# Optimization experiments

Measured on AMD Instinct MI355X. Metric: run time of the kernel, lower is better.

The kernel has to match this reference:

```python
import jax, jax.numpy as jnp
import numpy as np
from jax import lax

T = 131072  # num frames
PARENTS = [-1, 0, 0, 1, 2, 3, 4, 5, 6]          # lower-body kinematic tree
LOWER_BODY = [0, 1, 2, 4, 5, 7, 8, 10, 11]      # SMPL joint ids of the 9 lower-body joints
FEET = [7, 5, 8, 6]                              # left toe, left heel, right toe, right heel (lower-body local ids)
FLOOR_Y = -0.93                                  # min y of ankle/foot joints in SMPL zero pose
GRAVITY_VELOCITY = -0.0018


def setup_inputs() -> dict:
    key = jax.random.key(0)
    k1, k2, k3 = jax.random.split(key, 3)
    pose = jax.random.normal(k1, (T, 24, 3, 3), dtype=jnp.float32)
    bone = 0.2 * jax.random.normal(k2, (9, 3), dtype=jnp.float32)
    bone = bone.at[:3].set(0.0)  # root + hip offsets zeroed, as in __init__ (b[:3] = 0)
    index = jax.random.randint(k3, (T,), 0, 4, dtype=jnp.int32)
    return {"pose": pose, "lower_body_bone": bone, "index": index}


def _forward_kinematics(pose_lower, bone):
    # pose_lower: [T, 9, 3, 3] local rotations; bone: [9, 3] bone offsets.
    # R_global[i] = R_global[parent] @ R_local[i];  p[i] = p[parent] + R_global[parent] @ bone[i]
    Rg = [pose_lower[:, 0]]
    p = [jnp.broadcast_to(bone[0], (pose_lower.shape[0], 3))]
    for i in range(1, 9):
        pa = PARENTS[i]
        Rg.append(jnp.einsum('tij,tjk->tik', Rg[pa], pose_lower[:, i]))
        p.append(p[pa] + jnp.einsum('tij,j->ti', Rg[pa], bone[i]))
    return jnp.stack(p, axis=1)  # [T, 9, 3]


def reference(pose, lower_body_bone, index):
    gravity = jnp.array([0.0, GRAVITY_VELOCITY, 0.0], dtype=pose.dtype)
    pose_lower = pose[:, jnp.array(LOWER_BODY)]               # [T, 9, 3, 3]
    j = _forward_kinematics(pose_lower, lower_body_bone)      # [T, 9, 3]

    # per-foot velocities: j[t-1] - j[t], zero at t=0  -> [T, 4, 3]
    feet = j[:, jnp.array(FEET)]                              # [T, 4, 3]
    vel_full = jnp.concatenate([jnp.zeros((1, 4, 3), dtype=j.dtype), feet[:-1] - feet[1:]], axis=0)
    vel_select = jnp.take_along_axis(vel_full, index[:, None, None].astype(jnp.int32), axis=1)[:, 0]  # [T, 3]
    velocity = gravity + vel_select                           # [T, 3]

    # sequential floor-contact correction on the y component
    foot_min_y = jnp.min(j[:, 5:9, 1], axis=1)                # [T]

    def step(root_y, inp):
        vy, fmin = inp
        foot_y = root_y + fmin
        vy_new = jnp.where(foot_y + vy <= FLOOR_Y, FLOOR_Y - foot_y, vy)
        return root_y + vy_new, vy_new

    _, vy_all = lax.scan(step, jnp.asarray(0.0, dtype=j.dtype), (velocity[:, 1], foot_min_y))
    velocity = velocity.at[:, 1].set(vy_all)

    trans = jnp.cumsum(velocity, axis=0)                      # velocity_to_root_position
    return pose, trans
```

## Files before the change

kernel.cpp:

```cpp
#include <hip/hip_runtime.h>
#include <math.h>

#define T_TOTAL   131072
#define POSE_FLTS (131072 * 216)
#define BT        64
#define NU        (T_TOTAL / BT)
#define F4PB      (BT * 54)
#define TS_STR    73
#define TILE_F    72
#define FLOOR_YC  (-0.93f)
#define GRAV_Y    (-0.0018f)
#define NEG_INF   (-INFINITY)

typedef float floatx4 __attribute__((ext_vector_type(4)));


__device__ __forceinline__ void mat3mul(const float* A, const float* B, float* C) {
#pragma unroll
    for (int r = 0; r < 3; ++r) {
#pragma unroll
        for (int c = 0; c < 3; ++c) {
            C[r * 3 + c] = fmaf(A[r * 3 + 2], B[6 + c],
                           fmaf(A[r * 3 + 1], B[3 + c],
                                A[r * 3 + 0] * B[c]));
        }
    }
}

__device__ __forceinline__ void mva(const float* R, const float* b,
                                    const float* pin, float* pout) {
#pragma unroll
    for (int r = 0; r < 3; ++r) {
        pout[r] = pin[r] + fmaf(R[r * 3 + 2], b[2],
                            fmaf(R[r * 3 + 1], b[1], R[r * 3 + 0] * b[0]));
    }
}

__device__ __forceinline__ float sel_foot(const float f[12], int idx, int c) {
    float r = f[0 + c];
    r = (idx == 1) ? f[3 + c] : r;
    r = (idx == 2) ? f[6 + c] : r;
    r = (idx == 3) ? f[9 + c] : r;
    return r;
}

__device__ __forceinline__ void fk_core(const float* Pl,
                                        const float* __restrict__ bone,
                                        float feet[12], float* fmin) {
    const float* M0 = Pl + 0;
    const float* M1 = Pl + 9;
    const float* M2 = Pl + 18;
    const float* M3 = Pl + 28;
    const float* M4 = Pl + 37;
    const float* M5 = Pl + 51;
    const float* M6 = Pl + 60;

    float R1[9], R2[9], R3[9], R4[9], R5[9], R6[9];
    mat3mul(M0, M1, R1);
    mat3mul(M0, M2, R2);
    mat3mul(R1, M3, R3);
    mat3mul(R2, M4, R4);
    mat3mul(R3, M5, R5);
    mat3mul(R4, M6, R6);

    float p0[3] = {bone[0], bone[1], bone[2]};
    float p1[3], p2[3], p3[3], p4a[3], p5[3], p6[3], p7[3], p8[3];
    mva(M0, bone + 3,  p0, p1);
    mva(M0, bone + 6,  p0, p2);
    mva(R1, bone + 9,  p1, p3);
    mva(R2, bone + 12, p2, p4a);
    mva(R3, bone + 15, p3, p5);
    mva(R4, bone + 18, p4a, p6);
    mva(R5, bone + 21, p5, p7);
    mva(R6, bone + 24, p6, p8);

    feet[0] = p7[0]; feet[1]  = p7[1]; feet[2]  = p7[2];
    feet[3] = p5[0]; feet[4]  = p5[1]; feet[5]  = p5[2];
    feet[6] = p8[0]; feet[7]  = p8[1]; feet[8]  = p8[2];
    feet[9] = p6[0]; feet[10] = p6[1]; feet[11] = p6[2];
    *fmin = fminf(fminf(p5[1], p6[1]), fminf(p7[1], p8[1]));
}

__device__ __forceinline__ void fk_feet_col(const float* __restrict__ tile, int col,
                                            const float* __restrict__ bone,
                                            float feet[12], float* fmin) {
    float Pl[TILE_F];
    const float* p = tile + col * TS_STR;
#pragma unroll
    for (int f = 0; f < TILE_F; ++f) Pl[f] = p[f];
    fk_core(Pl, bone, feet, fmin);
}

__device__ __forceinline__ void wave_incl_scan(float& Sx, float& Sz,
                                               float& A, float& B, int lane) {
#pragma unroll
    for (int off = 1; off < 64; off <<= 1) {
        float ox = __shfl_up(Sx, off, 64);
        float oz = __shfl_up(Sz, off, 64);
        float oA = __shfl_up(A, off, 64);
        float oB = __shfl_up(B, off, 64);
        if (lane >= off) {
            Sx += ox;
            Sz += oz;
            B = fmaxf(oB + A, B);
            A = oA + A;
        }
    }
}

__device__ __forceinline__ void extract_tile(float* __restrict__ tile, int idx, floatx4 q) {
    int tsl = idx / 54;
    int w   = idx - tsl * 54;
    int base = -1;
    if (w <= 6)                  base = 4 * w;
    else if (w >= 9 && w <= 13)  base = 4 * w - 8;
    else if (w >= 15 && w <= 20) base = 4 * w - 12;
    if (base >= 0) {
        float* p = &tile[tsl * TS_STR + base];
        p[0] = q.x; p[1] = q.y; p[2] = q.z; p[3] = q.w;
    }
}


__global__ __launch_bounds__(256) void k_main(const float* __restrict__ pose,
                                              const float* __restrict__ bone,
                                              const int* __restrict__ index,
                                              floatx4* __restrict__ outPose4,
                                              float4* __restrict__ vws,
                                              float4* __restrict__ wsAgg) {
    __shared__ __align__(16) float tile[65 * TS_STR + 4];
    int tid = threadIdx.x, u = blockIdx.x;

    const floatx4* __restrict__ src = (const floatx4*)pose + (size_t)u * F4PB;
    floatx4*       __restrict__ dst = outPose4              + (size_t)u * F4PB;

    floatx4 r[14];
#pragma unroll
    for (int j = 0; j < 13; ++j) r[j] = src[j * 256 + tid];
    floatx4 qb;
    bool has14  = (tid < 128);
    bool hasBnd = (u > 0 && tid >= 128 && tid < 128 + 18);
    if (has14) {
        r[13] = src[13 * 256 + tid];
    } else if (hasBnd) {
        int k = tid - 128;
        int o = k + (k >= 7 ? 2 : 0) + (k >= 12 ? 1 : 0);
        qb = *(const floatx4*)(pose + ((size_t)u * BT - 1) * 216 + o * 4);
    }
    int idxv = 0;
    if (tid < 64) idxv = index[u * BT + tid];

#pragma unroll
    for (int j = 0; j < 13; ++j) {
        int idx = j * 256 + tid;
        __builtin_nontemporal_store(r[j], &dst[idx]);
        extract_tile(tile, idx, r[j]);
    }
    if (has14) {
        int idx = 13 * 256 + tid;
        __builtin_nontemporal_store(r[13], &dst[idx]);
        extract_tile(tile, idx, r[13]);
    } else if (hasBnd) {
        int k = tid - 128;
        float* p = &tile[64 * TS_STR + 4 * k];
#pragma unroll
        for (int i = 0; i < 4; ++i) p[i] = qb[i];
    }
    __syncthreads();

    if (tid < 64) {
        int lane = tid;
        int t = u * BT + lane;

        float feet[12], fmin;
        fk_feet_col(tile, lane, bone, feet, &fmin);

        float fb[12];
        if (lane == 0 && u > 0) {
            float mb;
            fk_feet_col(tile, 64, bone, fb, &mb);
        }

        float fp[12];
#pragma unroll
        for (int k = 0; k < 12; ++k) fp[k] = __shfl_up(feet[k], 1, 64);
        if (lane == 0 && u > 0) {
#pragma unroll
            for (int k = 0; k < 12; ++k) fp[k] = fb[k];
        }

        float vx, vy, vz;
        if (t == 0) {
            vx = 0.f; vy = GRAV_Y; vz = 0.f;
        } else {
            vx = sel_foot(fp, idxv, 0) - sel_foot(feet, idxv, 0);
            vy = GRAV_Y + sel_foot(fp, idxv, 1) - sel_foot(feet, idxv, 1);
            vz = sel_foot(fp, idxv, 2) - sel_foot(feet, idxv, 2);
        }
        float ix = vx, iz = vz, iA = vy, iB = FLOOR_YC - fmin;
        wave_incl_scan(ix, iz, iA, iB, lane);

        vws[(size_t)t] = make_float4(ix, iz, iA, iB);
        if (lane == 63) wsAgg[u] = make_float4(ix, iz, iA, iB);
    }
}


__global__ __launch_bounds__(256) void k_apply(const float4* __restrict__ wsAgg,
                                               const float4* __restrict__ vws,
                                               float* __restrict__ trans) {
    __shared__ float4 wtot[4];
    __shared__ float4 pre[4];
    int tid = threadIdx.x, bk = blockIdx.x;
    int lane = tid & 63, wv = tid >> 6;

    float4 a[8];
#pragma unroll
    for (int k = 0; k < 8; ++k) a[k] = wsAgg[tid * 8 + k];
    float cx = a[0].x, cz = a[0].y, ca = a[0].z, cb = a[0].w;
#pragma unroll
    for (int k = 1; k < 8; ++k) {
        cb = fmaxf(cb + a[k].z, a[k].w);
        ca += a[k].z;
        cx += a[k].x; cz += a[k].y;
    }

    float sx = cx, sz = cz, sa = ca, sb = cb;
    wave_incl_scan(sx, sz, sa, sb, lane);
    if (lane == 63) wtot[wv] = make_float4(sx, sz, sa, sb);

    float ex = __shfl_up(sx, 1, 64);
    float ez = __shfl_up(sz, 1, 64);
    float eA = __shfl_up(sa, 1, 64);
    float eB = __shfl_up(sb, 1, 64);
    if (lane == 0) { ex = 0.f; ez = 0.f; eA = 0.f; eB = NEG_INF; }
    __syncthreads();

    float wx = 0.f, wz = 0.f, wA = 0.f, wB = NEG_INF;
    for (int w = 0; w < wv; ++w) {
        float4 c = wtot[w];
        wx += c.x; wz += c.y;
        wB = fmaxf(wB + c.z, c.w);
        wA += c.z;
    }
    float tx = wx + ex, tz = wz + ez;
    float tB = fmaxf(wB + eA, eB);
    float tA = wA + eA;

    if (tid == (bk >> 1)) {
        int j0 = bk * 4 - tid * 8;
        float px = tx, pz = tz, pA = tA, pB = tB;
#pragma unroll
        for (int k = 0; k < 8; ++k) {
            if (k >= j0 && k < j0 + 4)
                pre[k - j0] = make_float4(px, pz, fmaxf(pA, pB), 0.f);
            pB = fmaxf(pB + a[k].z, a[k].w);
            pA += a[k].z;
            px += a[k].x; pz += a[k].y;
        }
    }
    __syncthreads();

    float4 bin = pre[wv];
    size_t t = ((size_t)bk * 4 + wv) * 64 + lane;
    float4 v = vws[t];
    trans[t * 3 + 0] = bin.x + v.x;
    trans[t * 3 + 1] = fmaxf(bin.z + v.z, v.w);
    trans[t * 3 + 2] = bin.y + v.y;
}


extern "C" void kernel_launch(void* const* d_in, const int* in_sizes, int n_in,
                              void* d_out, int out_size, void* d_ws, size_t ws_size,
                              hipStream_t stream) {
    const float* pose  = (const float*)d_in[0];
    const float* bone  = (const float*)d_in[1];
    const int*   index = (const int*)d_in[2];
    float* out   = (float*)d_out;
    float* trans = out + POSE_FLTS;

    float4* vws   = (float4*)d_ws;
    float4* wsAgg = vws + T_TOTAL;
    (void)ws_size; (void)n_in; (void)in_sizes; (void)out_size;

    k_main <<<NU, 256, 0, stream>>>(pose, bone, index, (floatx4*)out, vws, wsAgg);
    k_apply<<<NU / 4, 256, 0, stream>>>(wsAgg, vws, trans);
}
```

Before: 48.77 us.

## Specialize warps: copy waves stream pose, compute wave loads FK data directly

Splits each block into a copy role (three waves streaming the pose block to the output with nontemporal stores) and a compute role (one wave that loads its frame's 18 needed float4s straight from global memory and runs forward kinematics plus the wave scan). This removes the shared-memory tile, the extract scatter and the block barrier. In exchange the compute wave reads pose data a second time with strided per-lane 16-byte loads that are poorly coalesced, relying on cache hits. Every lane now also recomputes the boundary frame's FK when u>0, not just lane 0.

New measurement: 46.28 us, median of 2. 1.05x faster.

```diff
diff --git a/kernel.cpp b/kernel.cpp
--- a/kernel.cpp
+++ b/kernel.cpp
@@ -6,8 +6,6 @@
 #define BT        64
 #define NU        (T_TOTAL / BT)
 #define F4PB      (BT * 54)
-#define TS_STR    73
-#define TILE_F    72
 #define FLOOR_YC  (-0.93f)
 #define GRAV_Y    (-0.0018f)
 #define NEG_INF   (-INFINITY)
@@ -81,14 +79,17 @@
     *fmin = fminf(fminf(p5[1], p6[1]), fminf(p7[1], p8[1]));
 }
 
-__device__ __forceinline__ void fk_feet_col(const float* __restrict__ tile, int col,
-                                            const float* __restrict__ bone,
-                                            float feet[12], float* fmin) {
-    float Pl[TILE_F];
-    const float* p = tile + col * TS_STR;
-#pragma unroll
-    for (int f = 0; f < TILE_F; ++f) Pl[f] = p[f];
-    fk_core(Pl, bone, feet, fmin);
+__device__ __forceinline__ void load_compact(const floatx4* __restrict__ pp,
+                                             float Pl[72]) {
+#pragma unroll
+    for (int k = 0; k < 18; ++k) {
+        int o = k + (k >= 7 ? 2 : 0) + (k >= 12 ? 1 : 0);
+        floatx4 q = pp[o];
+        Pl[4 * k + 0] = q.x;
+        Pl[4 * k + 1] = q.y;
+        Pl[4 * k + 2] = q.z;
+        Pl[4 * k + 3] = q.w;
+    }
 }
 
 __device__ __forceinline__ void wave_incl_scan(float& Sx, float& Sz,
@@ -108,19 +109,6 @@
     }
 }
 
-__device__ __forceinline__ void extract_tile(float* __restrict__ tile, int idx, floatx4 q) {
-    int tsl = idx / 54;
-    int w   = idx - tsl * 54;
-    int base = -1;
-    if (w <= 6)                  base = 4 * w;
-    else if (w >= 9 && w <= 13)  base = 4 * w - 8;
-    else if (w >= 15 && w <= 20) base = 4 * w - 12;
-    if (base >= 0) {
-        float* p = &tile[tsl * TS_STR + base];
-        p[0] = q.x; p[1] = q.y; p[2] = q.z; p[3] = q.w;
-    }
-}
-
 
 __global__ __launch_bounds__(256) void k_main(const float* __restrict__ pose,
                                               const float* __restrict__ bone,
@@ -128,81 +116,63 @@
                                               floatx4* __restrict__ outPose4,
                                               float4* __restrict__ vws,
                                               float4* __restrict__ wsAgg) {
-    __shared__ __align__(16) float tile[65 * TS_STR + 4];
     int tid = threadIdx.x, u = blockIdx.x;
 
-    const floatx4* __restrict__ src = (const floatx4*)pose + (size_t)u * F4PB;
-    floatx4*       __restrict__ dst = outPose4              + (size_t)u * F4PB;
-
-    floatx4 r[14];
-#pragma unroll
-    for (int j = 0; j < 13; ++j) r[j] = src[j * 256 + tid];
-    floatx4 qb;
-    bool has14  = (tid < 128);
-    bool hasBnd = (u > 0 && tid >= 128 && tid < 128 + 18);
-    if (has14) {
-        r[13] = src[13 * 256 + tid];
-    } else if (hasBnd) {
-        int k = tid - 128;
-        int o = k + (k >= 7 ? 2 : 0) + (k >= 12 ? 1 : 0);
-        qb = *(const floatx4*)(pose + ((size_t)u * BT - 1) * 216 + o * 4);
-    }
-    int idxv = 0;
-    if (tid < 64) idxv = index[u * BT + tid];
-
-#pragma unroll
-    for (int j = 0; j < 13; ++j) {
-        int idx = j * 256 + tid;
-        __builtin_nontemporal_store(r[j], &dst[idx]);
-        extract_tile(tile, idx, r[j]);
-    }
-    if (has14) {
-        int idx = 13 * 256 + tid;
-        __builtin_nontemporal_store(r[13], &dst[idx]);
-        extract_tile(tile, idx, r[13]);
-    } else if (hasBnd) {
-        int k = tid - 128;
-        float* p = &tile[64 * TS_STR + 4 * k];
-#pragma unroll
-        for (int i = 0; i < 4; ++i) p[i] = qb[i];
-    }
-    __syncthreads();
-
-    if (tid < 64) {
-        int lane = tid;
-        int t = u * BT + lane;
-
-        float feet[12], fmin;
-        fk_feet_col(tile, lane, bone, feet, &fmin);
-
-        float fb[12];
-        if (lane == 0 && u > 0) {
-            float mb;
-            fk_feet_col(tile, 64, bone, fb, &mb);
-        }
-
-        float fp[12];
-#pragma unroll
-        for (int k = 0; k < 12; ++k) fp[k] = __shfl_up(feet[k], 1, 64);
-        if (lane == 0 && u > 0) {
-#pragma unroll
-            for (int k = 0; k < 12; ++k) fp[k] = fb[k];
-        }
-
-        float vx, vy, vz;
-        if (t == 0) {
-            vx = 0.f; vy = GRAV_Y; vz = 0.f;
-        } else {
-            vx = sel_foot(fp, idxv, 0) - sel_foot(feet, idxv, 0);
-            vy = GRAV_Y + sel_foot(fp, idxv, 1) - sel_foot(feet, idxv, 1);
-            vz = sel_foot(fp, idxv, 2) - sel_foot(feet, idxv, 2);
-        }
-        float ix = vx, iz = vz, iA = vy, iB = FLOOR_YC - fmin;
-        wave_incl_scan(ix, iz, iA, iB, lane);
-
-        vws[(size_t)t] = make_float4(ix, iz, iA, iB);
-        if (lane == 63) wsAgg[u] = make_float4(ix, iz, iA, iB);
-    }
+    if (tid >= 64) {
+        int tt = tid - 64;
+        const floatx4* __restrict__ src = (const floatx4*)pose + (size_t)u * F4PB;
+        floatx4*       __restrict__ dst = outPose4              + (size_t)u * F4PB;
+#pragma unroll
+        for (int bat = 0; bat < 2; ++bat) {
+            floatx4 r[9];
+#pragma unroll
+            for (int j = 0; j < 9; ++j)
+                r[j] = src[(bat * 9 + j) * 192 + tt];
+#pragma unroll
+            for (int j = 0; j < 9; ++j)
+                __builtin_nontemporal_store(r[j], &dst[(bat * 9 + j) * 192 + tt]);
+        }
+        return;
+    }
+
+    int lane = tid;
+    int t = u * BT + lane;
+    int idxv = index[t];
+
+    float Pl[72];
+    load_compact((const floatx4*)(pose + (size_t)t * 216), Pl);
+
+    float fb[12];
+    if (u > 0) {
+        float Pb[72], mb;
+        load_compact((const floatx4*)(pose + ((size_t)u * BT - 1) * 216), Pb);
+        fk_core(Pb, bone, fb, &mb);
+    }
+
+    float feet[12], fmin;
+    fk_core(Pl, bone, feet, &fmin);
+
+    float fp[12];
+#pragma unroll
+    for (int k = 0; k < 12; ++k) fp[k] = __shfl_up(feet[k], 1, 64);
+    if (lane == 0 && u > 0) {
+#pragma unroll
+        for (int k = 0; k < 12; ++k) fp[k] = fb[k];
+    }
+
+    float vx, vy, vz;
+    if (t == 0) {
+        vx = 0.f; vy = GRAV_Y; vz = 0.f;
+    } else {
+        vx = sel_foot(fp, idxv, 0) - sel_foot(feet, idxv, 0);
+        vy = GRAV_Y + sel_foot(fp, idxv, 1) - sel_foot(feet, idxv, 1);
+        vz = sel_foot(fp, idxv, 2) - sel_foot(feet, idxv, 2);
+    }
+    float ix = vx, iz = vz, iA = vy, iB = FLOOR_YC - fmin;
+    wave_incl_scan(ix, iz, iA, iB, lane);
+
+    vws[(size_t)t] = make_float4(ix, iz, iA, iB);
+    if (lane == 63) wsAgg[u] = make_float4(ix, iz, iA, iB);
 }
 
 
```
